# Kernel tuning notes

Hardware: AMD Instinct MI355X
Metric: run time of the kernel (lower is better)

## Reference

```python
import jax, jax.numpy as jnp
import numpy as np

B, S, H = 2, 4096, 256
NH, NKV = 8, 4
HD = H // NH          # 32
GROUPS = NH // NKV    # 2
ROPE_BASE = 10000.0


def _rope_cos_sin(seq_len, dim, dtype):
    inv_freq = 1.0 / (ROPE_BASE ** (jnp.arange(0, dim, 2, dtype=jnp.float32) / dim))
    t = jnp.arange(seq_len, dtype=jnp.float32)
    freqs = jnp.outer(t, inv_freq)            # [S, dim/2]
    emb = jnp.concatenate([freqs, freqs], -1)  # [S, dim]
    return jnp.cos(emb).astype(dtype), jnp.sin(emb).astype(dtype)


def _rotate_half(x):
    x1, x2 = jnp.split(x, 2, axis=-1)
    return jnp.concatenate([-x2, x1], axis=-1)


def setup_inputs() -> dict:
    key = jax.random.key(0)
    k0, k1, k2, k3, k4 = jax.random.split(key, 5)
    return {
        "hidden_states": jax.random.normal(k0, (B, S, H), jnp.float32),
        "Wq": jax.random.normal(k1, (H, H), jnp.float32) * 0.02,
        "Wk": jax.random.normal(k2, (NKV * HD, H), jnp.float32) * 0.02,
        "Wv": jax.random.normal(k3, (NKV * HD, H), jnp.float32) * 0.02,
        "Wo": jax.random.normal(k4, (H, H), jnp.float32) * 0.02,
    }


def reference(hidden_states, Wq, Wk, Wv, Wo):
    b, s, _ = hidden_states.shape
    # projections (nn.Linear: x @ W.T)
    q = (hidden_states @ Wq.T).reshape(b, s, NH, HD).transpose(0, 2, 1, 3)   # [b,nh,s,hd]
    k = (hidden_states @ Wk.T).reshape(b, s, NKV, HD).transpose(0, 2, 1, 3)  # [b,nkv,s,hd]
    v = (hidden_states @ Wv.T).reshape(b, s, NKV, HD).transpose(0, 2, 1, 3)
    # RoPE
    cos, sin = _rope_cos_sin(s, HD, hidden_states.dtype)  # [s,hd]
    q = q * cos + _rotate_half(q) * sin
    k = k * cos + _rotate_half(k) * sin
    # GQA: repeat kv heads (repeat_interleave over head dim)
    k = jnp.repeat(k, GROUPS, axis=1)  # [b,nh,s,hd]
    v = jnp.repeat(v, GROUPS, axis=1)
    # scores + causal mask
    scores = jnp.einsum('bhqd,bhkd->bhqk', q, k) / jnp.sqrt(jnp.float32(HD)).astype(q.dtype)
    causal = jnp.triu(jnp.full((s, s), -jnp.inf, dtype=scores.dtype), k=1)
    scores = scores + causal
    attn = jax.nn.softmax(scores.astype(jnp.float32), axis=-1).astype(q.dtype)
    out = jnp.einsum('bhqk,bhkd->bhqd', attn, v)          # [b,nh,s,hd]
    out = out.transpose(0, 2, 1, 3).reshape(b, s, NH * HD)
    return out @ Wo.T
```

## Files before the change

### kernel.cpp

```cpp
#include <hip/hip_runtime.h>
#include <hip/hip_bf16.h>
#include <stdint.h>

#define NB 2
#define SEQ 4096
#define HID 256
#define NHEAD 8
#define NKVH 4
#define HDIM 32

typedef __bf16 bf16;
typedef __bf16 bf16x8 __attribute__((ext_vector_type(8)));
typedef float f32x4 __attribute__((ext_vector_type(4)));

static __device__ __forceinline__ uint16_t bfbits(float f) {
    bf16 h = (bf16)f;
    return __builtin_bit_cast(uint16_t, h);
}
static __device__ __forceinline__ uint32_t pack_bf16(float lo, float hi) {
    return (uint32_t)bfbits(lo) | ((uint32_t)bfbits(hi) << 16);
}
static __device__ __forceinline__ float fexp2(float x) {
#if __has_builtin(__builtin_amdgcn_exp2f)
    return __builtin_amdgcn_exp2f(x);
#else
    float r; asm("v_exp_f32 %0, %1" : "=v"(r) : "v"(x)); return r;
#endif
}
static __device__ __forceinline__ void gld_lds16(const void* g, void* l) {
    __builtin_amdgcn_global_load_lds(
        (const __attribute__((address_space(1))) void*)g,
        (__attribute__((address_space(3))) void*)l, 16, 0, 0);
}

__global__ __launch_bounds__(256) void qkv_proj(
    const float* __restrict__ hs, const float* __restrict__ Wq,
    const float* __restrict__ Wk, const float* __restrict__ Wv,
    bf16* __restrict__ qws, bf16* __restrict__ kws, bf16* __restrict__ vtws)
{
    __shared__ bf16 As[64][136];
    __shared__ bf16 Bs[64][136];
    const int t = threadIdx.x;
    const int wid = t >> 6, lane = t & 63;
    const int g = lane >> 4, c = lane & 15;
    const int n0 = blockIdx.x * 64;
    const int m0 = blockIdx.y * 64;

    const float* bsrc; int ro;
    if (n0 < 256)      { bsrc = Wq; ro = n0; }
    else if (n0 < 384) { bsrc = Wk; ro = n0 - 256; }
    else               { bsrc = Wv; ro = n0 - 384; }

    const f32x4 zf = {0.f, 0.f, 0.f, 0.f};
    f32x4 acc[4] = {zf, zf, zf, zf};

    const int c4 = t & 31;
    const int rb = t >> 5;

    for (int ks = 0; ks < 256; ks += 128) {
        __syncthreads();
        #pragma unroll
        for (int i = 0; i < 8; ++i) {
            int row = i * 8 + rb;
            float4 v = *(const float4*)&hs[(size_t)(m0 + row) * HID + ks + c4 * 4];
            ushort4 w; w.x = bfbits(v.x); w.y = bfbits(v.y); w.z = bfbits(v.z); w.w = bfbits(v.w);
            *(ushort4*)&As[row][c4 * 4] = w;
        }
        #pragma unroll
        for (int i = 0; i < 8; ++i) {
            int row = i * 8 + rb;
            float4 v = *(const float4*)&bsrc[(size_t)(ro + row) * HID + ks + c4 * 4];
            ushort4 w; w.x = bfbits(v.x); w.y = bfbits(v.y); w.z = bfbits(v.z); w.w = bfbits(v.w);
            *(ushort4*)&Bs[row][c4 * 4] = w;
        }
        __syncthreads();
        #pragma unroll
        for (int kk = 0; kk < 128; kk += 32) {
            bf16x8 af = *(const bf16x8*)&As[wid * 16 + c][kk + g * 8];
            #pragma unroll
            for (int nt = 0; nt < 4; ++nt) {
                bf16x8 bfr = *(const bf16x8*)&Bs[nt * 16 + c][kk + g * 8];
                acc[nt] = __builtin_amdgcn_mfma_f32_16x16x32_bf16(af, bfr, acc[nt], 0, 0, 0);
            }
        }
    }

    const float qscale = 1.4426950408889634f * 0.17677669529663687f;
    const float invf = exp2f(-0.83048202372184f * (float)c);
    #pragma unroll
    for (int r = 0; r < 4; ++r) {
        int m = m0 + wid * 16 + g * 4 + r;
        int b = m >> 12, s = m & (SEQ - 1);
        float sn, cs;
        sincosf((float)s * invf, &sn, &cs);
        if (n0 < 256) {
            #pragma unroll
            for (int np = 0; np < 4; np += 2) {
                int h = (n0 + np * 16) >> 5;
                float x1 = acc[np][r], x2 = acc[np + 1][r];
                float y1 = (x1 * cs - x2 * sn) * qscale;
                float y2 = (x2 * cs + x1 * sn) * qscale;
                size_t base = ((size_t)(b * NHEAD + h) * SEQ + s) * HDIM;
                qws[base + c] = (bf16)y1;
                qws[base + 16 + c] = (bf16)y2;
            }
        } else if (n0 < 384) {
            #pragma unroll
            for (int np = 0; np < 4; np += 2) {
                int kh = (n0 - 256 + np * 16) >> 5;
                float x1 = acc[np][r], x2 = acc[np + 1][r];
                float y1 = x1 * cs - x2 * sn;
                float y2 = x2 * cs + x1 * sn;
                size_t base = ((size_t)(b * NKVH + kh) * SEQ + s) * HDIM;
                kws[base + c] = (bf16)y1;
                kws[base + 16 + c] = (bf16)y2;
            }
        } else {
            #pragma unroll
            for (int nt = 0; nt < 4; ++nt) {
                int ng = n0 + nt * 16 + c - 384;
                int vh = ng >> 5, d = ng & 31;
                vtws[((size_t)(b * NKVH + vh) * HDIM + d) * SEQ + s] = (bf16)acc[nt][r];
            }
        }
    }
}

template<int SPLIT>
__global__ __launch_bounds__(256, 2) void attn_fwd(
    const bf16* __restrict__ qws, const bf16* __restrict__ kws,
    const bf16* __restrict__ vtws, bf16* __restrict__ att,
    float* __restrict__ Oa, float* __restrict__ Ob,
    float* __restrict__ la, float* __restrict__ lb)
{
    __shared__ bf16 Kb[2][64 * 32];
    __shared__ bf16 Vb[2][32 * 64];
    __shared__ float tr[4][16 * 33];
    const int t = threadIdx.x;
    const int w = t >> 6, lane = t & 63;
    const int g = lane >> 4, c = lane & 15;
    const int wg = blockIdx.x;
    const int h = wg & 7;
    int T, b, half;
    if (SPLIT) {
        const int rest = wg >> 3;
        half = rest & 1;
        const int r2 = rest >> 1;
        b = r2 & 1;
        T = 31 - (r2 >> 1);
    } else {
        const int rest = wg >> 3;
        half = 0;
        b = rest & 1;
        T = 31 - (rest >> 1);
    }
    const int kvh = h >> 1;
    const bf16* Kg = kws + (size_t)(b * NKVH + kvh) * SEQ * HDIM;
    const bf16* Vg = vtws + (size_t)(b * NKVH + kvh) * HDIM * SEQ;
    const int cbase = SPLIT ? half * (T + 1) : 0;
    const int nloc = SPLIT ? (T + 1) : (2 * T + 2);
    const int q0 = T * 128 + w * 32;
    const int d_w = 2 * T + (w >> 1);

    const bf16* Qb = qws + (size_t)(b * NHEAD + h) * SEQ * HDIM;
    bf16x8 qf0 = *(const bf16x8*)&Qb[(size_t)(q0 + c) * HDIM + g * 8];
    bf16x8 qf1 = *(const bf16x8*)&Qb[(size_t)(q0 + 16 + c) * HDIM + g * 8];

    const int sd = t >> 3, sseg = t & 7;
    const bf16* kg_t = Kg + t * 8;
    const bf16* vg_t = Vg + (size_t)sd * SEQ + (sseg ^ (sd & 7)) * 8;
    char* kl[2] = { (char*)&Kb[0][0] + w * 1024, (char*)&Kb[1][0] + w * 1024 };
    char* vl[2] = { (char*)&Vb[0][0] + w * 1024, (char*)&Vb[1][0] + w * 1024 };

    const int kperm = 8 * (c >> 2) + (c & 3);
    const int kro = kperm * 64 + g * 16;
    const int cx = c & 7;
    const int vro0 = c * 128, vro1 = (16 + c) * 128;

    const f32x4 zf = {0.f, 0.f, 0.f, 0.f};
    union { uint32_t u[4]; bf16x8 v; } onesf;
    onesf.u[0] = onesf.u[1] = onesf.u[2] = onesf.u[3] = 0x3F803F80u;

    f32x4 o00 = zf, o01 = zf, ol0 = zf;
    f32x4 o10 = zf, o11 = zf, ol1 = zf;

    gld_lds16(kg_t + (size_t)cbase * 2048, kl[0]);
    gld_lds16(vg_t + (size_t)cbase * 64, vl[0]);
    __syncthreads();

    #pragma unroll 1
    for (int s = 0; s < nloc; ++s) {
        const int ci = cbase + s;
        const int sn = s + 1;
        if (sn < nloc) {
            gld_lds16(kg_t + (size_t)(cbase + sn) * 2048, kl[sn & 1]);
            gld_lds16(vg_t + (size_t)(cbase + sn) * 64, vl[sn & 1]);
        }
        if (ci <= d_w) {
            const char* kbuf = (const char*)&Kb[s & 1][0];
            const char* vbuf = (const char*)&Vb[s & 1][0];

            bf16x8 kf0 = *(const bf16x8*)(kbuf + kro);
            bf16x8 kf1 = *(const bf16x8*)(kbuf + kro + 256);
            bf16x8 kf2 = *(const bf16x8*)(kbuf + kro + 2048);
            bf16x8 kf3 = *(const bf16x8*)(kbuf + kro + 2304);
            bf16x8 vf00 = *(const bf16x8*)(vbuf + vro0 + ((g ^ cx) << 4));
            bf16x8 vf01 = *(const bf16x8*)(vbuf + vro1 + ((g ^ cx) << 4));
            bf16x8 vf10 = *(const bf16x8*)(vbuf + vro0 + (((4 + g) ^ cx) << 4));
            bf16x8 vf11 = *(const bf16x8*)(vbuf + vro1 + (((4 + g) ^ cx) << 4));

            const bool diag = (ci == d_w);
            const int qbase = (w & 1) * 32 + c;

            {
                f32x4 st0 = __builtin_amdgcn_mfma_f32_16x16x32_bf16(kf0, qf0, zf, 0, 0, 0);
                f32x4 st1 = __builtin_amdgcn_mfma_f32_16x16x32_bf16(kf1, qf0, zf, 0, 0, 0);
                f32x4 st2 = __builtin_amdgcn_mfma_f32_16x16x32_bf16(kf2, qf0, zf, 0, 0, 0);
                f32x4 st3 = __builtin_amdgcn_mfma_f32_16x16x32_bf16(kf3, qf0, zf, 0, 0, 0);
                if (diag) {
                    const int qoff = qbase;
                    #pragma unroll
                    for (int r = 0; r < 4; ++r) {
                        if (8 * g + r > qoff)          st0[r] = -1e30f;
                        if (8 * g + 4 + r > qoff)      st1[r] = -1e30f;
                        if (32 + 8 * g + r > qoff)     st2[r] = -1e30f;
                        if (32 + 8 * g + 4 + r > qoff) st3[r] = -1e30f;
                    }
                }
                float p00 = fexp2(st0[0]), p01 = fexp2(st0[1]), p02 = fexp2(st0[2]), p03 = fexp2(st0[3]);
                float p10 = fexp2(st1[0]), p11 = fexp2(st1[1]), p12 = fexp2(st1[2]), p13 = fexp2(st1[3]);
                float p20 = fexp2(st2[0]), p21 = fexp2(st2[1]), p22 = fexp2(st2[2]), p23 = fexp2(st2[3]);
                float p30 = fexp2(st3[0]), p31 = fexp2(st3[1]), p32 = fexp2(st3[2]), p33 = fexp2(st3[3]);
                union { uint32_t u[4]; bf16x8 v; } pb0, pb1;
                asm("v_cvt_pk_bf16_f32 %0, %1, %2" : "=v"(pb0.u[0]) : "v"(p00), "v"(p01));
                asm("v_cvt_pk_bf16_f32 %0, %1, %2" : "=v"(pb0.u[1]) : "v"(p02), "v"(p03));
                asm("v_cvt_pk_bf16_f32 %0, %1, %2" : "=v"(pb0.u[2]) : "v"(p10), "v"(p11));
                asm("v_cvt_pk_bf16_f32 %0, %1, %2" : "=v"(pb0.u[3]) : "v"(p12), "v"(p13));
                asm("v_cvt_pk_bf16_f32 %0, %1, %2" : "=v"(pb1.u[0]) : "v"(p20), "v"(p21));
                asm("v_cvt_pk_bf16_f32 %0, %1, %2" : "=v"(pb1.u[1]) : "v"(p22), "v"(p23));
                asm("v_cvt_pk_bf16_f32 %0, %1, %2" : "=v"(pb1.u[2]) : "v"(p30), "v"(p31));
                asm("v_cvt_pk_bf16_f32 %0, %1, %2" : "=v"(pb1.u[3]) : "v"(p32), "v"(p33));
                o00 = __builtin_amdgcn_mfma_f32_16x16x32_bf16(vf00, pb0.v, o00, 0, 0, 0);
                o01 = __builtin_amdgcn_mfma_f32_16x16x32_bf16(vf01, pb0.v, o01, 0, 0, 0);
                ol0 = __builtin_amdgcn_mfma_f32_16x16x32_bf16(onesf.v, pb0.v, ol0, 0, 0, 0);
                o00 = __builtin_amdgcn_mfma_f32_16x16x32_bf16(vf10, pb1.v, o00, 0, 0, 0);
                o01 = __builtin_amdgcn_mfma_f32_16x16x32_bf16(vf11, pb1.v, o01, 0, 0, 0);
                ol0 = __builtin_amdgcn_mfma_f32_16x16x32_bf16(onesf.v, pb1.v, ol0, 0, 0, 0);
            }
            {
                f32x4 st0 = __builtin_amdgcn_mfma_f32_16x16x32_bf16(kf0, qf1, zf, 0, 0, 0);
                f32x4 st1 = __builtin_amdgcn_mfma_f32_16x16x32_bf16(kf1, qf1, zf, 0, 0, 0);
                f32x4 st2 = __builtin_amdgcn_mfma_f32_16x16x32_bf16(kf2, qf1, zf, 0, 0, 0);
                f32x4 st3 = __builtin_amdgcn_mfma_f32_16x16x32_bf16(kf3, qf1, zf, 0, 0, 0);
                if (diag) {
                    const int qoff = qbase + 16;
                    #pragma unroll
                    for (int r = 0; r < 4; ++r) {
                        if (8 * g + r > qoff)          st0[r] = -1e30f;
                        if (8 * g + 4 + r > qoff)      st1[r] = -1e30f;
                        if (32 + 8 * g + r > qoff)     st2[r] = -1e30f;
                        if (32 + 8 * g + 4 + r > qoff) st3[r] = -1e30f;
                    }
                }
                float p00 = fexp2(st0[0]), p01 = fexp2(st0[1]), p02 = fexp2(st0[2]), p03 = fexp2(st0[3]);
                float p10 = fexp2(st1[0]), p11 = fexp2(st1[1]), p12 = fexp2(st1[2]), p13 = fexp2(st1[3]);
                float p20 = fexp2(st2[0]), p21 = fexp2(st2[1]), p22 = fexp2(st2[2]), p23 = fexp2(st2[3]);
                float p30 = fexp2(st3[0]), p31 = fexp2(st3[1]), p32 = fexp2(st3[2]), p33 = fexp2(st3[3]);
                union { uint32_t u[4]; bf16x8 v; } pb0, pb1;
                asm("v_cvt_pk_bf16_f32 %0, %1, %2" : "=v"(pb0.u[0]) : "v"(p00), "v"(p01));
                asm("v_cvt_pk_bf16_f32 %0, %1, %2" : "=v"(pb0.u[1]) : "v"(p02), "v"(p03));
                asm("v_cvt_pk_bf16_f32 %0, %1, %2" : "=v"(pb0.u[2]) : "v"(p10), "v"(p11));
                asm("v_cvt_pk_bf16_f32 %0, %1, %2" : "=v"(pb0.u[3]) : "v"(p12), "v"(p13));
                asm("v_cvt_pk_bf16_f32 %0, %1, %2" : "=v"(pb1.u[0]) : "v"(p20), "v"(p21));
                asm("v_cvt_pk_bf16_f32 %0, %1, %2" : "=v"(pb1.u[1]) : "v"(p22), "v"(p23));
                asm("v_cvt_pk_bf16_f32 %0, %1, %2" : "=v"(pb1.u[2]) : "v"(p30), "v"(p31));
                asm("v_cvt_pk_bf16_f32 %0, %1, %2" : "=v"(pb1.u[3]) : "v"(p32), "v"(p33));
                o10 = __builtin_amdgcn_mfma_f32_16x16x32_bf16(vf00, pb0.v, o10, 0, 0, 0);
                o11 = __builtin_amdgcn_mfma_f32_16x16x32_bf16(vf01, pb0.v, o11, 0, 0, 0);
                ol1 = __builtin_amdgcn_mfma_f32_16x16x32_bf16(onesf.v, pb0.v, ol1, 0, 0, 0);
                o10 = __builtin_amdgcn_mfma_f32_16x16x32_bf16(vf10, pb1.v, o10, 0, 0, 0);
                o11 = __builtin_amdgcn_mfma_f32_16x16x32_bf16(vf11, pb1.v, o11, 0, 0, 0);
                ol1 = __builtin_amdgcn_mfma_f32_16x16x32_bf16(onesf.v, pb1.v, ol1, 0, 0, 0);
            }
        }
        __syncthreads();
    }

    #pragma unroll 1
    for (int j = 0; j < 2; ++j) {
        f32x4 a0 = j ? o10 : o00;
        f32x4 a1 = j ? o11 : o01;
        f32x4 al = j ? ol1 : ol0;
        if (SPLIT) {
            #pragma unroll
            for (int r = 0; r < 4; ++r) {
                tr[w][c * 33 + 4 * g + r]      = a0[r];
                tr[w][c * 33 + 16 + 4 * g + r] = a1[r];
            }
            float* Op = half ? Ob : Oa;
            float* lp = half ? lb : la;
            if (g == 0) lp[((size_t)b * SEQ + q0 + j * 16 + c) * 8 + h] = al[0];
            int q = lane >> 2, dp = (lane & 3) * 8;
            size_t m = (size_t)b * SEQ + q0 + j * 16 + q;
            float4 f0 = make_float4(tr[w][q * 33 + dp + 0], tr[w][q * 33 + dp + 1],
                                    tr[w][q * 33 + dp + 2], tr[w][q * 33 + dp + 3]);
            float4 f1 = make_float4(tr[w][q * 33 + dp + 4], tr[w][q * 33 + dp + 5],
                                    tr[w][q * 33 + dp + 6], tr[w][q * 33 + dp + 7]);
            *(float4*)&Op[m * HID + h * HDIM + dp]     = f0;
            *(float4*)&Op[m * HID + h * HDIM + dp + 4] = f1;
        } else {
            float inv = 1.0f / al[0];
            #pragma unroll
            for (int r = 0; r < 4; ++r) {
                tr[w][c * 33 + 4 * g + r]      = a0[r] * inv;
                tr[w][c * 33 + 16 + 4 * g + r] = a1[r] * inv;
            }
            int q = lane >> 2, dp = (lane & 3) * 8;
            uint32_t u0 = pack_bf16(tr[w][q * 33 + dp + 0], tr[w][q * 33 + dp + 1]);
            uint32_t u1 = pack_bf16(tr[w][q * 33 + dp + 2], tr[w][q * 33 + dp + 3]);
            uint32_t u2 = pack_bf16(tr[w][q * 33 + dp + 4], tr[w][q * 33 + dp + 5]);
            uint32_t u3 = pack_bf16(tr[w][q * 33 + dp + 6], tr[w][q * 33 + dp + 7]);
            size_t base = ((size_t)b * SEQ + q0 + j * 16 + q) * HID + h * HDIM + dp;
            *(uint4*)&att[base] = make_uint4(u0, u1, u2, u3);
        }
    }
}

__global__ __launch_bounds__(256) void combine(
    const float* __restrict__ Oa, const float* __restrict__ Ob,
    const float* __restrict__ la, const float* __restrict__ lb,
    bf16* __restrict__ att)
{
    const size_t e = ((size_t)blockIdx.x * 256 + threadIdx.x) * 8;
    const size_t m = e >> 8;
    const int hh = (int)(e & 255) >> 5;
    const float inv = 1.0f / (la[m * 8 + hh] + lb[m * 8 + hh]);
    float4 a0 = *(const float4*)&Oa[e];
    float4 a1 = *(const float4*)&Oa[e + 4];
    float4 b0 = *(const float4*)&Ob[e];
    float4 b1 = *(const float4*)&Ob[e + 4];
    uint32_t u0 = pack_bf16((a0.x + b0.x) * inv, (a0.y + b0.y) * inv);
    uint32_t u1 = pack_bf16((a0.z + b0.z) * inv, (a0.w + b0.w) * inv);
    uint32_t u2 = pack_bf16((a1.x + b1.x) * inv, (a1.y + b1.y) * inv);
    uint32_t u3 = pack_bf16((a1.z + b1.z) * inv, (a1.w + b1.w) * inv);
    *(uint4*)&att[e] = make_uint4(u0, u1, u2, u3);
}

__global__ __launch_bounds__(256) void out_proj(
    const bf16* __restrict__ att, const float* __restrict__ Wo,
    float* __restrict__ out)
{
    __shared__ bf16 As[64][136];
    __shared__ bf16 Bs[64][136];
    const int t = threadIdx.x;
    const int wid = t >> 6, lane = t & 63;
    const int g = lane >> 4, c = lane & 15;
    const int n0 = blockIdx.x * 64;
    const int m0 = blockIdx.y * 64;

    const f32x4 zf = {0.f, 0.f, 0.f, 0.f};
    f32x4 acc[4] = {zf, zf, zf, zf};

    const int c4 = t & 31;
    const int rb = t >> 5;

    for (int ks = 0; ks < 256; ks += 128) {
        __syncthreads();
        #pragma unroll
        for (int i = 0; i < 8; ++i) {
            int row = i * 8 + rb;
            ushort4 v = *(const ushort4*)&att[(size_t)(m0 + row) * HID + ks + c4 * 4];
            *(ushort4*)&As[row][c4 * 4] = v;
        }
        #pragma unroll
        for (int i = 0; i < 8; ++i) {
            int row = i * 8 + rb;
            float4 v = *(const float4*)&Wo[(size_t)(n0 + row) * HID + ks + c4 * 4];
            ushort4 w; w.x = bfbits(v.x); w.y = bfbits(v.y); w.z = bfbits(v.z); w.w = bfbits(v.w);
            *(ushort4*)&Bs[row][c4 * 4] = w;
        }
        __syncthreads();
        #pragma unroll
        for (int kk = 0; kk < 128; kk += 32) {
            bf16x8 af = *(const bf16x8*)&As[wid * 16 + c][kk + g * 8];
            #pragma unroll
            for (int nt = 0; nt < 4; ++nt) {
                bf16x8 bfr = *(const bf16x8*)&Bs[nt * 16 + c][kk + g * 8];
                acc[nt] = __builtin_amdgcn_mfma_f32_16x16x32_bf16(af, bfr, acc[nt], 0, 0, 0);
            }
        }
    }

    #pragma unroll
    for (int nt = 0; nt < 4; ++nt) {
        #pragma unroll
        for (int r = 0; r < 4; ++r) {
            int m = m0 + wid * 16 + g * 4 + r;
            out[(size_t)m * HID + n0 + nt * 16 + c] = acc[nt][r];
        }
    }
}

extern "C" void kernel_launch(void* const* d_in, const int* in_sizes, int n_in,
                              void* d_out, int out_size, void* d_ws, size_t ws_size,
                              hipStream_t stream) {
    const float* hs = (const float*)d_in[0];
    const float* Wq = (const float*)d_in[1];
    const float* Wk = (const float*)d_in[2];
    const float* Wv = (const float*)d_in[3];
    const float* Wo = (const float*)d_in[4];
    char* ws = (char*)d_ws;
    bf16* qws  = (bf16*)(ws);
    bf16* kws  = (bf16*)(ws + 4194304);
    bf16* vtws = (bf16*)(ws + 6291456);
    bf16* att  = (bf16*)(ws + 8388608);
    float* Oa  = (float*)(ws + 12582912);
    float* Ob  = (float*)(ws + 20971520);
    float* la  = (float*)(ws + 29360128);
    float* lb  = (float*)(ws + 29622272);
    const bool split = (ws_size >= 29884416);

    qkv_proj<<<dim3(8, 128), 256, 0, stream>>>(hs, Wq, Wk, Wv, qws, kws, vtws);
    if (split) {
        attn_fwd<1><<<1024, 256, 0, stream>>>(qws, kws, vtws, att, Oa, Ob, la, lb);
        combine<<<1024, 256, 0, stream>>>(Oa, Ob, la, lb, att);
        out_proj<<<dim3(4, 128), 256, 0, stream>>>(att, Wo, (float*)d_out);
    } else {
        attn_fwd<0><<<512, 256, 0, stream>>>(qws, kws, vtws, att, Oa, Ob, la, lb);
        out_proj<<<dim3(4, 128), 256, 0, stream>>>(att, Wo, (float*)d_out);
    }
}
```

Before: 63.19 us.

## Pre-convert inputs to bf16 and load GEMM tiles via direct global-to-LDS

Adds a separate conversion kernel that casts hidden states and all weight matrices to bf16 in the workspace. The QKV and output projections then load the full K=256 tiles with global_load_lds into XOR-swizzled shared memory, using one sync instead of a two-pass convert-and-store loop. The attention path is fixed to the split variant with a combine step. This adds a kernel launch and an extra round trip of hidden states through memory, and it now requires a larger workspace without checking ws_size, in exchange for cheaper, asynchronous tile loads.

```diff
diff --git a/kernel.cpp b/kernel.cpp
--- a/kernel.cpp
+++ b/kernel.cpp
@@ -33,63 +33,76 @@
         (__attribute__((address_space(3))) void*)l, 16, 0, 0);
 }
 
-__global__ __launch_bounds__(256) void qkv_proj(
+__global__ __launch_bounds__(256) void to_bf16(
     const float* __restrict__ hs, const float* __restrict__ Wq,
     const float* __restrict__ Wk, const float* __restrict__ Wv,
+    const float* __restrict__ Wo,
+    bf16* __restrict__ hsb, bf16* __restrict__ Wb, bf16* __restrict__ Wob)
+{
+    size_t idx = ((size_t)blockIdx.x * 256 + threadIdx.x) * 8;
+    const float* src; bf16* dst; size_t off;
+    if (idx < 2097152)      { src = hs; dst = hsb;        off = idx; }
+    else if (idx < 2162688) { src = Wq; dst = Wb;         off = idx - 2097152; }
+    else if (idx < 2195456) { src = Wk; dst = Wb + 65536; off = idx - 2162688; }
+    else if (idx < 2228224) { src = Wv; dst = Wb + 98304; off = idx - 2195456; }
+    else                    { src = Wo; dst = Wob;        off = idx - 2228224; }
+    float4 a = *(const float4*)&src[off];
+    float4 b = *(const float4*)&src[off + 4];
+    uint32_t u0 = pack_bf16(a.x, a.y);
+    uint32_t u1 = pack_bf16(a.z, a.w);
+    uint32_t u2 = pack_bf16(b.x, b.y);
+    uint32_t u3 = pack_bf16(b.z, b.w);
+    *(uint4*)&dst[off] = make_uint4(u0, u1, u2, u3);
+}
+
+__global__ __launch_bounds__(256, 2) void qkv2(
+    const bf16* __restrict__ hsb, const bf16* __restrict__ Wb,
     bf16* __restrict__ qws, bf16* __restrict__ kws, bf16* __restrict__ vtws)
 {
-    __shared__ bf16 As[64][136];
-    __shared__ bf16 Bs[64][136];
+    __shared__ bf16 As[64 * 256];
+    __shared__ bf16 Bs[64 * 256];
     const int t = threadIdx.x;
     const int wid = t >> 6, lane = t & 63;
     const int g = lane >> 4, c = lane & 15;
     const int n0 = blockIdx.x * 64;
     const int m0 = blockIdx.y * 64;
 
-    const float* bsrc; int ro;
-    if (n0 < 256)      { bsrc = Wq; ro = n0; }
-    else if (n0 < 384) { bsrc = Wk; ro = n0 - 256; }
-    else               { bsrc = Wv; ro = n0 - 384; }
+    {
+        const int half = lane >> 5;
+        const int seg = lane & 31;
+        #pragma unroll
+        for (int i = 0; i < 8; ++i) {
+            const int row = (i * 4 + wid) * 2 + half;
+            const int sseg = seg ^ (row & 7);
+            gld_lds16(hsb + (size_t)(m0 + row) * 256 + sseg * 8,
+                      (char*)As + wid * 1024 + i * 4096);
+            gld_lds16(Wb + (size_t)(n0 + row) * 256 + sseg * 8,
+                      (char*)Bs + wid * 1024 + i * 4096);
+        }
+    }
+    __syncthreads();
 
     const f32x4 zf = {0.f, 0.f, 0.f, 0.f};
     f32x4 acc[4] = {zf, zf, zf, zf};
-
-    const int c4 = t & 31;
-    const int rb = t >> 5;
-
-    for (int ks = 0; ks < 256; ks += 128) {
-        __syncthreads();
-        #pragma unroll
-        for (int i = 0; i < 8; ++i) {
-            int row = i * 8 + rb;
-            float4 v = *(const float4*)&hs[(size_t)(m0 + row) * HID + ks + c4 * 4];
-            ushort4 w; w.x = bfbits(v.x); w.y = bfbits(v.y); w.z = bfbits(v.z); w.w = bfbits(v.w);
-            *(ushort4*)&As[row][c4 * 4] = w;
-        }
-        #pragma unroll
-        for (int i = 0; i < 8; ++i) {
-            int row = i * 8 + rb;
-            float4 v = *(const float4*)&bsrc[(size_t)(ro + row) * HID + ks + c4 * 4];
-            ushort4 w; w.x = bfbits(v.x); w.y = bfbits(v.y); w.z = bfbits(v.z); w.w = bfbits(v.w);
-            *(ushort4*)&Bs[row][c4 * 4] = w;
-        }
-        __syncthreads();
-        #pragma unroll
-        for (int kk = 0; kk < 128; kk += 32) {
-            bf16x8 af = *(const bf16x8*)&As[wid * 16 + c][kk + g * 8];
-            #pragma unroll
-            for (int nt = 0; nt < 4; ++nt) {
-                bf16x8 bfr = *(const bf16x8*)&Bs[nt * 16 + c][kk + g * 8];
-                acc[nt] = __builtin_amdgcn_mfma_f32_16x16x32_bf16(af, bfr, acc[nt], 0, 0, 0);
-            }
+    const int r = wid * 16 + c;
+    const int aBase = r * 512;
+    const int s7 = c & 7;
+    #pragma unroll
+    for (int j = 0; j < 8; ++j) {
+        const int so = ((4 * j + g) ^ s7) << 4;
+        bf16x8 af = *(const bf16x8*)((const char*)As + aBase + so);
+        #pragma unroll
+        for (int nt = 0; nt < 4; ++nt) {
+            bf16x8 bfr = *(const bf16x8*)((const char*)Bs + (nt * 16 + c) * 512 + so);
+            acc[nt] = __builtin_amdgcn_mfma_f32_16x16x32_bf16(af, bfr, acc[nt], 0, 0, 0);
         }
     }
 
     const float qscale = 1.4426950408889634f * 0.17677669529663687f;
     const float invf = exp2f(-0.83048202372184f * (float)c);
     #pragma unroll
-    for (int r = 0; r < 4; ++r) {
-        int m = m0 + wid * 16 + g * 4 + r;
+    for (int rr = 0; rr < 4; ++rr) {
+        int m = m0 + wid * 16 + g * 4 + rr;
         int b = m >> 12, s = m & (SEQ - 1);
         float sn, cs;
         sincosf((float)s * invf, &sn, &cs);
@@ -97,7 +110,7 @@
             #pragma unroll
             for (int np = 0; np < 4; np += 2) {
                 int h = (n0 + np * 16) >> 5;
-                float x1 = acc[np][r], x2 = acc[np + 1][r];
+                float x1 = acc[np][rr], x2 = acc[np + 1][rr];
                 float y1 = (x1 * cs - x2 * sn) * qscale;
                 float y2 = (x2 * cs + x1 * sn) * qscale;
                 size_t base = ((size_t)(b * NHEAD + h) * SEQ + s) * HDIM;
@@ -108,7 +121,7 @@
             #pragma unroll
             for (int np = 0; np < 4; np += 2) {
                 int kh = (n0 - 256 + np * 16) >> 5;
-                float x1 = acc[np][r], x2 = acc[np + 1][r];
+                float x1 = acc[np][rr], x2 = acc[np + 1][rr];
                 float y1 = x1 * cs - x2 * sn;
                 float y2 = x2 * cs + x1 * sn;
                 size_t base = ((size_t)(b * NKVH + kh) * SEQ + s) * HDIM;
@@ -120,16 +133,15 @@
             for (int nt = 0; nt < 4; ++nt) {
                 int ng = n0 + nt * 16 + c - 384;
                 int vh = ng >> 5, d = ng & 31;
-                vtws[((size_t)(b * NKVH + vh) * HDIM + d) * SEQ + s] = (bf16)acc[nt][r];
+                vtws[((size_t)(b * NKVH + vh) * HDIM + d) * SEQ + s] = (bf16)acc[nt][rr];
             }
         }
     }
 }
 
-template<int SPLIT>
 __global__ __launch_bounds__(256, 2) void attn_fwd(
     const bf16* __restrict__ qws, const bf16* __restrict__ kws,
-    const bf16* __restrict__ vtws, bf16* __restrict__ att,
+    const bf16* __restrict__ vtws,
     float* __restrict__ Oa, float* __restrict__ Ob,
     float* __restrict__ la, float* __restrict__ lb)
 {
@@ -141,24 +153,16 @@
     const int g = lane >> 4, c = lane & 15;
     const int wg = blockIdx.x;
     const int h = wg & 7;
-    int T, b, half;
-    if (SPLIT) {
-        const int rest = wg >> 3;
-        half = rest & 1;
-        const int r2 = rest >> 1;
-        b = r2 & 1;
-        T = 31 - (r2 >> 1);
-    } else {
-        const int rest = wg >> 3;
-        half = 0;
-        b = rest & 1;
-        T = 31 - (rest >> 1);
-    }
+    const int rest = wg >> 3;
+    const int half = rest & 1;
+    const int r2 = rest >> 1;
+    const int b = r2 & 1;
+    const int T = 31 - (r2 >> 1);
     const int kvh = h >> 1;
     const bf16* Kg = kws + (size_t)(b * NKVH + kvh) * SEQ * HDIM;
     const bf16* Vg = vtws + (size_t)(b * NKVH + kvh) * HDIM * SEQ;
-    const int cbase = SPLIT ? half * (T + 1) : 0;
-    const int nloc = SPLIT ? (T + 1) : (2 * T + 2);
+    const int cbase = half * (T + 1);
+    const int nloc = T + 1;
     const int q0 = T * 128 + w * 32;
     const int d_w = 2 * T + (w >> 1);
 
@@ -220,11 +224,11 @@
                 if (diag) {
                     const int qoff = qbase;
                     #pragma unroll
-                    for (int r = 0; r < 4; ++r) {
-                        if (8 * g + r > qoff)          st0[r] = -1e30f;
-                        if (8 * g + 4 + r > qoff)      st1[r] = -1e30f;
-                        if (32 + 8 * g + r > qoff)     st2[r] = -1e30f;
-                        if (32 + 8 * g + 4 + r > qoff) st3[r] = -1e30f;
+                    for (int rr = 0; rr < 4; ++rr) {
+                        if (8 * g + rr > qoff)          st0[rr] = -1e30f;
+                        if (8 * g + 4 + rr > qoff)      st1[rr] = -1e30f;
+                        if (32 + 8 * g + rr > qoff)     st2[rr] = -1e30f;
+                        if (32 + 8 * g + 4 + rr > qoff) st3[rr] = -1e30f;
                     }
                 }
                 float p00 = fexp2(st0[0]), p01 = fexp2(st0[1]), p02 = fexp2(st0[2]), p03 = fexp2(st0[3]);
@@ -255,11 +259,11 @@
                 if (diag) {
                     const int qoff = qbase + 16;
                     #pragma unroll
-                    for (int r = 0; r < 4; ++r) {
-                        if (8 * g + r > qoff)          st0[r] = -1e30f;
-                        if (8 * g + 4 + r > qoff)      st1[r] = -1e30f;
-                        if (32 + 8 * g + r > qoff)     st2[r] = -1e30f;
-                        if (32 + 8 * g + 4 + r > qoff) st3[r] = -1e30f;
+                    for (int rr = 0; rr < 4; ++rr) {
+                        if (8 * g + rr > qoff)          st0[rr] = -1e30f;
+                        if (8 * g + 4 + rr > qoff)      st1[rr] = -1e30f;
+                        if (32 + 8 * g + rr > qoff)     st2[rr] = -1e30f;
+                        if (32 + 8 * g + 4 + rr > qoff) st3[rr] = -1e30f;
                     }
                 }
                 float p00 = fexp2(st0[0]), p01 = fexp2(st0[1]), p02 = fexp2(st0[2]), p03 = fexp2(st0[3]);
@@ -291,38 +295,22 @@
         f32x4 a0 = j ? o10 : o00;
         f32x4 a1 = j ? o11 : o01;
         f32x4 al = j ? ol1 : ol0;
-        if (SPLIT) {
-            #pragma unroll
-            for (int r = 0; r < 4; ++r) {
-                tr[w][c * 33 + 4 * g + r]      = a0[r];
-                tr[w][c * 33 + 16 + 4 * g + r] = a1[r];
-            }
-            float* Op = half ? Ob : Oa;
-            float* lp = half ? lb : la;
-            if (g == 0) lp[((size_t)b * SEQ + q0 + j * 16 + c) * 8 + h] = al[0];
-            int q = lane >> 2, dp = (lane & 3) * 8;
-            size_t m = (size_t)b * SEQ + q0 + j * 16 + q;
-            float4 f0 = make_float4(tr[w][q * 33 + dp + 0], tr[w][q * 33 + dp + 1],
-                                    tr[w][q * 33 + dp + 2], tr[w][q * 33 + dp + 3]);
-            float4 f1 = make_float4(tr[w][q * 33 + dp + 4], tr[w][q * 33 + dp + 5],
-                                    tr[w][q * 33 + dp + 6], tr[w][q * 33 + dp + 7]);
-            *(float4*)&Op[m * HID + h * HDIM + dp]     = f0;
-            *(float4*)&Op[m * HID + h * HDIM + dp + 4] = f1;
-        } else {
-            float inv = 1.0f / al[0];
-            #pragma unroll
-            for (int r = 0; r < 4; ++r) {
-                tr[w][c * 33 + 4 * g + r]      = a0[r] * inv;
-                tr[w][c * 33 + 16 + 4 * g + r] = a1[r] * inv;
-            }
-            int q = lane >> 2, dp = (lane & 3) * 8;
-            uint32_t u0 = pack_bf16(tr[w][q * 33 + dp + 0], tr[w][q * 33 + dp + 1]);
-            uint32_t u1 = pack_bf16(tr[w][q * 33 + dp + 2], tr[w][q * 33 + dp + 3]);
-            uint32_t u2 = pack_bf16(tr[w][q * 33 + dp + 4], tr[w][q * 33 + dp + 5]);
-            uint32_t u3 = pack_bf16(tr[w][q * 33 + dp + 6], tr[w][q * 33 + dp + 7]);
-            size_t base = ((size_t)b * SEQ + q0 + j * 16 + q) * HID + h * HDIM + dp;
-            *(uint4*)&att[base] = make_uint4(u0, u1, u2, u3);
-        }
+        #pragma unroll
+        for (int rr = 0; rr < 4; ++rr) {
+            tr[w][c * 33 + 4 * g + rr]      = a0[rr];
+            tr[w][c * 33 + 16 + 4 * g + rr] = a1[rr];
+        }
+        float* Op = half ? Ob : Oa;
+        float* lp = half ? lb : la;
+        if (g == 0) lp[((size_t)b * SEQ + q0 + j * 16 + c) * 8 + h] = al[0];
+        int q = lane >> 2, dp = (lane & 3) * 8;
+        size_t m = (size_t)b * SEQ + q0 + j * 16 + q;
+        float4 f0 = make_float4(tr[w][q * 33 + dp + 0], tr[w][q * 33 + dp + 1],
+                                tr[w][q * 33 + dp + 2], tr[w][q * 33 + dp + 3]);
+        float4 f1 = make_float4(tr[w][q * 33 + dp + 4], tr[w][q * 33 + dp + 5],
+                                tr[w][q * 33 + dp + 6], tr[w][q * 33 + dp + 7]);
+        *(float4*)&Op[m * HID + h * HDIM + dp]     = f0;
+        *(float4*)&Op[m * HID + h * HDIM + dp + 4] = f1;
     }
 }
 
@@ -346,57 +334,55 @@
     *(uint4*)&att[e] = make_uint4(u0, u1, u2, u3);
 }
 
-__global__ __launch_bounds__(256) void out_proj(
-    const bf16* __restrict__ att, const float* __restrict__ Wo,
+__global__ __launch_bounds__(256, 2) void out_proj2(
+    const bf16* __restrict__ att, const bf16* __restrict__ Wob,
     float* __restrict__ out)
 {
-    __shared__ bf16 As[64][136];
-    __shared__ bf16 Bs[64][136];
+    __shared__ bf16 As[64 * 256];
+    __shared__ bf16 Bs[64 * 256];
     const int t = threadIdx.x;
     const int wid = t >> 6, lane = t & 63;
     const int g = lane >> 4, c = lane & 15;
     const int n0 = blockIdx.x * 64;
     const int m0 = blockIdx.y * 64;
 
+    {
+        const int half = lane >> 5;
+        const int seg = lane & 31;
+        #pragma unroll
+        for (int i = 0; i < 8; ++i) {
+            const int row = (i * 4 + wid) * 2 + half;
+            const int sseg = seg ^ (row & 7);
+            gld_lds16(att + (size_t)(m0 + row) * 256 + sseg * 8,
+                      (char*)As + wid * 1024 + i * 4096);
+            gld_lds16(Wob + (size_t)(n0 + row) * 256 + sseg * 8,
+                      (char*)Bs + wid * 1024 + i * 4096);
+        }
+    }
+    __syncthreads();
+
     const f32x4 zf = {0.f, 0.f, 0.f, 0.f};
     f32x4 acc[4] = {zf, zf, zf, zf};
-
-    const int c4 = t & 31;
-    const int rb = t >> 5;
-
-    for (int ks = 0; ks < 256; ks += 128) {
-        __syncthreads();
-        #pragma unroll
-        for (int i = 0; i < 8; ++i) {
-            int row = i * 8 + rb;
-            ushort4 v = *(const ushort4*)&att[(size_t)(m0 + row) * HID + ks + c4 * 4];
-            *(ushort4*)&As[row][c4 * 4] = v;
-        }
-        #pragma unroll
-        for (int i = 0; i < 8; ++i) {
-            int row = i * 8 + rb;
-            float4 v = *(const float4*)&Wo[(size_t)(n0 + row) * HID + ks + c4 * 4];
-            ushort4 w; w.x = bfbits(v.x); w.y = bfbits(v.y); w.z = bfbits(v.z); w.w = bfbits(v.w);
-            *(ushort4*)&Bs[row][c4 * 4] = w;
-        }
-        __syncthreads();
-        #pragma unroll
-        for (int kk = 0; kk < 128; kk += 32) {
-            bf16x8 af = *(const bf16x8*)&As[wid * 16 + c][kk + g * 8];
-            #pragma unroll
-            for (int nt = 0; nt < 4; ++nt) {
-                bf16x8 bfr = *(const bf16x8*)&Bs[nt * 16 + c][kk + g * 8];
-                acc[nt] = __builtin_amdgcn_mfma_f32_16x16x32_bf16(af, bfr, acc[nt], 0, 0, 0);
-            }
+    const int r = wid * 16 + c;
+    const int aBase = r * 512;
+    const int s7 = c & 7;
+    #pragma unroll
+    for (int j = 0; j < 8; ++j) {
+        const int so = ((4 * j + g) ^ s7) << 4;
+        bf16x8 af = *(const bf16x8*)((const char*)As + aBase + so);
+        #pragma unroll
+        for (int nt = 0; nt < 4; ++nt) {
+            bf16x8 bfr = *(const bf16x8*)((const char*)Bs + (nt * 16 + c) * 512 + so);
+            acc[nt] = __builtin_amdgcn_mfma_f32_16x16x32_bf16(af, bfr, acc[nt], 0, 0, 0);
         }
     }
 
     #pragma unroll
     for (int nt = 0; nt < 4; ++nt) {
         #pragma unroll
-        for (int r = 0; r < 4; ++r) {
-            int m = m0 + wid * 16 + g * 4 + r;
-            out[(size_t)m * HID + n0 + nt * 16 + c] = acc[nt][r];
+        for (int rr = 0; rr < 4; ++rr) {
+            int m = m0 + wid * 16 + g * 4 + rr;
+            out[(size_t)m * HID + n0 + nt * 16 + c] = acc[nt][rr];
         }
     }
 }
@@ -418,15 +404,13 @@
     float* Ob  = (float*)(ws + 20971520);
     float* la  = (float*)(ws + 29360128);
     float* lb  = (float*)(ws + 29622272);
-    const bool split = (ws_size >= 29884416);
-
-    qkv_proj<<<dim3(8, 128), 256, 0, stream>>>(hs, Wq, Wk, Wv, qws, kws, vtws);
-    if (split) {
-        attn_fwd<1><<<1024, 256, 0, stream>>>(qws, kws, vtws, att, Oa, Ob, la, lb);
-        combine<<<1024, 256, 0, stream>>>(Oa, Ob, la, lb, att);
-        out_proj<<<dim3(4, 128), 256, 0, stream>>>(att, Wo, (float*)d_out);
-    } else {
-        attn_fwd<0><<<512, 256, 0, stream>>>(qws, kws, vtws, att, Oa, Ob, la, lb);
-        out_proj<<<dim3(4, 128), 256, 0, stream>>>(att, Wo, (float*)d_out);
-    }
-}
+    bf16* hsb  = (bf16*)(ws + 29884416);
+    bf16* Wb   = (bf16*)(ws + 34078720);
+    bf16* Wob  = (bf16*)(ws + 34340864);
+
+    to_bf16<<<1120, 256, 0, stream>>>(hs, Wq, Wk, Wv, Wo, hsb, Wb, Wob);
+    qkv2<<<dim3(8, 128), 256, 0, stream>>>(hsb, Wb, qws, kws, vtws);
+    attn_fwd<<<1024, 256, 0, stream>>>(qws, kws, vtws, Oa, Ob, la, lb);
+    combine<<<1024, 256, 0, stream>>>(Oa, Ob, la, lb, att);
+    out_proj2<<<dim3(4, 128), 256, 0, stream>>>(att, Wob, (float*)d_out);
+}
```

Measured after the change: 62.93 us. About the same (-0.4%).
